# Performance work log

Hardware: AMD Instinct MI355X
Metric: run time of the kernel (lower is better)

Reference implementation:

```python
import jax, jax.numpy as jnp
import numpy as np

KH, KW = 7, 7            # full kernel after pad_w reflect of the (4,4) half-kernel
SIGMA_COLOR = 0.1


def extract_patches(x, kh, kw):
    """Per-pixel kh x kw neighborhoods with reflect padding.
    x: (B,C,H,W) -> (B,C,H,W,K) with K = kh*kw, k = i*kw + j (row-major),
    matching torch unfold(2,..).unfold(3,..).flatten(-2) ordering."""
    top, left = (kh - 1) // 2, (kw - 1) // 2
    xp = jnp.pad(x, ((0, 0), (0, 0), (top, kh - 1 - top), (left, kw - 1 - left)), mode='reflect')
    B, C, H, W = x.shape
    return jnp.stack([xp[:, :, i:i + H, j:j + W] for i in range(kh) for j in range(kw)], axis=-1)


def setup_inputs() -> dict:
    key = jax.random.key(0)
    k1, k2, k3 = jax.random.split(key, 3)
    B, C, H, W = 2, 3, 512, 512
    x = jax.random.uniform(k1, (B, C, H, W), dtype=jnp.float32)
    guidance = jax.random.uniform(k2, (B, C, H, W), dtype=jnp.float32)
    # learnable half-kernel logits, one per pixel (num_boxes = H*W with box=(1,1))
    w0 = jax.random.normal(k3, (B, H * W, KH // 2 + 1, KW // 2 + 1), dtype=jnp.float32)
    return {"x": x, "guidance": guidance, "w0": w0}


def reference(x, guidance, w0):
    B, C, H, W = x.shape
    K = KH * KW
    # pad_w: reflect-pad the stored (4,4) half-kernel back to the full (7,7) kernel
    w = jnp.pad(w0, ((0, 0), (0, 0), (0, KH // 2), (0, KW // 2)), mode='reflect')
    # softmax over the flattened kernel taps, per pixel
    sw = jax.nn.softmax(w.reshape(B, H, W, K), axis=-1)                     # (B,H,W,K)
    # bilateral color kernel: squared L1(channel) distance patch-vs-center
    gp = extract_patches(guidance, KH, KW)                                  # (B,C,H,W,K)
    dist = jnp.square(jnp.abs(gp - guidance[..., None]).sum(axis=1))        # (B,H,W,K)
    color = jnp.nan_to_num(jnp.exp((-0.5 / SIGMA_COLOR ** 2) * dist), nan=0.0)
    wt = sw * color                                                         # (B,H,W,K)
    # weighted local average, normalized by total weight
    xp = extract_patches(x, KH, KW)                                         # (B,C,H,W,K)
    num = jnp.einsum('bchwk,bhwk->bchw', xp, wt)
    den = wt.sum(axis=-1)[:, None]                                          # (B,1,H,W)
    return (num / den).astype(jnp.float32)
```

## Files before the change

kernel.cpp:

```cpp
#include <hip/hip_runtime.h>

#define TILE_W 32
#define TILE_H 8
#define HALO 3
#define SW_ (TILE_W + 2*HALO)
#define SH_ (TILE_H + 2*HALO)
#define H_IMG 512
#define W_IMG 512
#define C_IMG 3

__device__ __forceinline__ int reflect_idx(int q, int n) {
    q = (q < 0) ? -q : q;
    q = (q >= n) ? (2 * n - 2 - q) : q;
    return q;
}

__global__ __launch_bounds__(256) void AdaptiveFilter_71416716198124_kernel(
    const float* __restrict__ x,
    const float* __restrict__ g,
    const float* __restrict__ w0,
    float* __restrict__ out)
{
    __shared__ float sg[C_IMG][SH_][SW_];
    __shared__ float sx[C_IMG][SH_][SW_];

    const int b  = blockIdx.z;
    const int h0 = blockIdx.y * TILE_H;
    const int w0c = blockIdx.x * TILE_W;
    const int tid = threadIdx.y * TILE_W + threadIdx.x;

    const int plane = H_IMG * W_IMG;
    const float* gb = g + (size_t)b * C_IMG * plane;
    const float* xb = x + (size_t)b * C_IMG * plane;

    for (int idx = tid; idx < C_IMG * SH_ * SW_; idx += TILE_W * TILE_H) {
        int c = idx / (SH_ * SW_);
        int r = idx - c * (SH_ * SW_);
        int sh = r / SW_;
        int sw = r - sh * SW_;
        int gh = reflect_idx(h0 + sh - HALO, H_IMG);
        int gw = reflect_idx(w0c + sw - HALO, W_IMG);
        int off = c * plane + gh * W_IMG + gw;
        sg[c][sh][sw] = gb[off];
        sx[c][sh][sw] = xb[off];
    }
    __syncthreads();

    const int lx = threadIdx.x, ly = threadIdx.y;
    const int h = h0 + ly, w = w0c + lx;

    const float4* wp = (const float4*)(w0 + ((size_t)((b * plane) + h * W_IMG + w) << 4));
    float4 a0 = wp[0], a1 = wp[1], a2 = wp[2], a3 = wp[3];
    float wv[16] = {a0.x, a0.y, a0.z, a0.w, a1.x, a1.y, a1.z, a1.w,
                    a2.x, a2.y, a2.z, a2.w, a3.x, a3.y, a3.z, a3.w};
    float mx = wv[0];
    #pragma unroll
    for (int i = 1; i < 16; i++) mx = fmaxf(mx, wv[i]);

    const float gc0 = sg[0][ly + HALO][lx + HALO];
    const float gc1 = sg[1][ly + HALO][lx + HALO];
    const float gc2 = sg[2][ly + HALO][lx + HALO];

    float n0 = 0.f, n1 = 0.f, n2 = 0.f, den = 0.f;
    #pragma unroll
    for (int i = 0; i < 7; i++) {
        const int mi = (i < 4) ? i : 6 - i;
        #pragma unroll
        for (int j = 0; j < 7; j++) {
            const int mj = (j < 4) ? j : 6 - j;
            float d0 = fabsf(sg[0][ly + i][lx + j] - gc0);
            float d1 = fabsf(sg[1][ly + i][lx + j] - gc1);
            float d2 = fabsf(sg[2][ly + i][lx + j] - gc2);
            float s = d0 + d1 + d2;
            float wt = __expf(wv[mi * 4 + mj] - mx - 50.0f * (s * s));
            n0 = fmaf(sx[0][ly + i][lx + j], wt, n0);
            n1 = fmaf(sx[1][ly + i][lx + j], wt, n1);
            n2 = fmaf(sx[2][ly + i][lx + j], wt, n2);
            den += wt;
        }
    }
    const float inv = 1.0f / den;
    size_t ob = (size_t)b * C_IMG * plane + (size_t)h * W_IMG + w;
    out[ob]             = n0 * inv;
    out[ob + plane]     = n1 * inv;
    out[ob + 2 * plane] = n2 * inv;
}

extern "C" void kernel_launch(void* const* d_in, const int* in_sizes, int n_in,
                              void* d_out, int out_size, void* d_ws, size_t ws_size,
                              hipStream_t stream) {
    const float* x  = (const float*)d_in[0];
    const float* g  = (const float*)d_in[1];
    const float* w0 = (const float*)d_in[2];
    float* out = (float*)d_out;

    dim3 block(TILE_W, TILE_H, 1);
    dim3 grid(W_IMG / TILE_W, H_IMG / TILE_H, 2);
    AdaptiveFilter_71416716198124_kernel<<<grid, block, 0, stream>>>(x, g, w0, out);
}
```

Measured before the change: 94.41 us.

## Compute four horizontal pixels per thread with vectorized shared-memory row reuse

Each thread now produces four adjacent output pixels instead of one. For each kernel row it loads 12 contiguous guidance and input values per channel from shared memory as float4s and reuses them across the four pixels' 7 taps, then writes the outputs as float4. The tile becomes 64x16 with a padded 72-wide shared row, and the max subtraction is folded into the logits before the loop. This cuts LDS traffic and instruction count per pixel. In exchange it raises register pressure and leaves fewer blocks to fill the GPU. The per-thread w0 loads are now strided by 64 bytes across lanes, which may hurt coalescing.

```diff
diff --git a/kernel.cpp b/kernel.cpp
--- a/kernel.cpp
+++ b/kernel.cpp
@@ -1,13 +1,16 @@
 #include <hip/hip_runtime.h>
 
-#define TILE_W 32
-#define TILE_H 8
+#define TPX 4
+#define BX 16
+#define BY 16
+#define TILE_W (BX*TPX)
+#define TILE_H BY
 #define HALO 3
-#define SW_ (TILE_W + 2*HALO)
-#define SH_ (TILE_H + 2*HALO)
+#define SW_V (TILE_W + 2*HALO)
+#define SROW 72
+#define SH_T (TILE_H + 2*HALO)
 #define H_IMG 512
 #define W_IMG 512
-#define C_IMG 3
 
 __device__ __forceinline__ int reflect_idx(int q, int n) {
     q = (q < 0) ? -q : q;
@@ -21,23 +24,22 @@
     const float* __restrict__ w0,
     float* __restrict__ out)
 {
-    __shared__ float sg[C_IMG][SH_][SW_];
-    __shared__ float sx[C_IMG][SH_][SW_];
+    __shared__ __align__(16) float sg[3][SH_T][SROW];
+    __shared__ __align__(16) float sx[3][SH_T][SROW];
 
-    const int b  = blockIdx.z;
-    const int h0 = blockIdx.y * TILE_H;
+    const int b   = blockIdx.z;
+    const int h0  = blockIdx.y * TILE_H;
     const int w0c = blockIdx.x * TILE_W;
-    const int tid = threadIdx.y * TILE_W + threadIdx.x;
+    const int tid = threadIdx.y * BX + threadIdx.x;
+    const int plane = H_IMG * W_IMG;
+    const float* gb = g + (size_t)b * 3 * plane;
+    const float* xb = x + (size_t)b * 3 * plane;
 
-    const int plane = H_IMG * W_IMG;
-    const float* gb = g + (size_t)b * C_IMG * plane;
-    const float* xb = x + (size_t)b * C_IMG * plane;
-
-    for (int idx = tid; idx < C_IMG * SH_ * SW_; idx += TILE_W * TILE_H) {
-        int c = idx / (SH_ * SW_);
-        int r = idx - c * (SH_ * SW_);
-        int sh = r / SW_;
-        int sw = r - sh * SW_;
+    for (int idx = tid; idx < 3 * SH_T * SW_V; idx += BX * BY) {
+        int c  = idx / (SH_T * SW_V);
+        int r  = idx - c * (SH_T * SW_V);
+        int sh = r / SW_V;
+        int sw = r - sh * SW_V;
         int gh = reflect_idx(h0 + sh - HALO, H_IMG);
         int gw = reflect_idx(w0c + sw - HALO, W_IMG);
         int off = c * plane + gh * W_IMG + gw;
@@ -46,44 +48,106 @@
     }
     __syncthreads();
 
-    const int lx = threadIdx.x, ly = threadIdx.y;
-    const int h = h0 + ly, w = w0c + lx;
+    const int lx4 = threadIdx.x * TPX;
+    const int ly  = threadIdx.y;
+    const int h   = h0 + ly;
+    const int wb  = w0c + lx4;
 
-    const float4* wp = (const float4*)(w0 + ((size_t)((b * plane) + h * W_IMG + w) << 4));
-    float4 a0 = wp[0], a1 = wp[1], a2 = wp[2], a3 = wp[3];
-    float wv[16] = {a0.x, a0.y, a0.z, a0.w, a1.x, a1.y, a1.z, a1.w,
-                    a2.x, a2.y, a2.z, a2.w, a3.x, a3.y, a3.z, a3.w};
-    float mx = wv[0];
+    float lw[TPX][16];
     #pragma unroll
-    for (int i = 1; i < 16; i++) mx = fmaxf(mx, wv[i]);
+    for (int p = 0; p < TPX; p++) {
+        const float4* wp = (const float4*)(w0 +
+            (((size_t)b * plane + (size_t)h * W_IMG + (wb + p)) << 4));
+        float4 a0 = wp[0], a1 = wp[1], a2 = wp[2], a3 = wp[3];
+        float v[16] = {a0.x,a0.y,a0.z,a0.w, a1.x,a1.y,a1.z,a1.w,
+                       a2.x,a2.y,a2.z,a2.w, a3.x,a3.y,a3.z,a3.w};
+        float mx = v[0];
+        #pragma unroll
+        for (int k = 1; k < 16; k++) mx = fmaxf(mx, v[k]);
+        #pragma unroll
+        for (int k = 0; k < 16; k++) lw[p][k] = v[k] - mx;
+    }
 
-    const float gc0 = sg[0][ly + HALO][lx + HALO];
-    const float gc1 = sg[1][ly + HALO][lx + HALO];
-    const float gc2 = sg[2][ly + HALO][lx + HALO];
+    float gc[TPX][3];
+    #pragma unroll
+    for (int p = 0; p < TPX; p++)
+        #pragma unroll
+        for (int c = 0; c < 3; c++)
+            gc[p][c] = sg[c][ly + HALO][lx4 + HALO + p];
 
-    float n0 = 0.f, n1 = 0.f, n2 = 0.f, den = 0.f;
+    float acc[TPX][3] = {};
+    float den[TPX] = {};
+
     #pragma unroll
     for (int i = 0; i < 7; i++) {
-        const int mi = (i < 4) ? i : 6 - i;
+        const int mi4 = ((i < 4) ? i : 6 - i) * 4;
+
+        float sd[TPX][7];
         #pragma unroll
-        for (int j = 0; j < 7; j++) {
-            const int mj = (j < 4) ? j : 6 - j;
-            float d0 = fabsf(sg[0][ly + i][lx + j] - gc0);
-            float d1 = fabsf(sg[1][ly + i][lx + j] - gc1);
-            float d2 = fabsf(sg[2][ly + i][lx + j] - gc2);
-            float s = d0 + d1 + d2;
-            float wt = __expf(wv[mi * 4 + mj] - mx - 50.0f * (s * s));
-            n0 = fmaf(sx[0][ly + i][lx + j], wt, n0);
-            n1 = fmaf(sx[1][ly + i][lx + j], wt, n1);
-            n2 = fmaf(sx[2][ly + i][lx + j], wt, n2);
-            den += wt;
+        for (int p = 0; p < TPX; p++)
+            #pragma unroll
+            for (int j = 0; j < 7; j++) sd[p][j] = 0.f;
+
+        #pragma unroll
+        for (int c = 0; c < 3; c++) {
+            const float4* pg = (const float4*)&sg[c][ly + i][lx4];
+            float4 g0 = pg[0], g1 = pg[1], g2 = pg[2];
+            float rg[12] = {g0.x,g0.y,g0.z,g0.w, g1.x,g1.y,g1.z,g1.w,
+                            g2.x,g2.y,g2.z,g2.w};
+            #pragma unroll
+            for (int p = 0; p < TPX; p++) {
+                const float cc = gc[p][c];
+                #pragma unroll
+                for (int j = 0; j < 7; j++)
+                    sd[p][j] += fabsf(rg[p + j] - cc);
+            }
+        }
+
+        #pragma unroll
+        for (int p = 0; p < TPX; p++) {
+            #pragma unroll
+            for (int j = 0; j < 7; j++) {
+                const int mj = (j < 4) ? j : 6 - j;
+                const float s = sd[p][j];
+                sd[p][j] = __expf(fmaf(-50.0f * s, s, lw[p][mi4 + mj]));
+            }
+        }
+
+        #pragma unroll
+        for (int c = 0; c < 3; c++) {
+            const float4* px = (const float4*)&sx[c][ly + i][lx4];
+            float4 x0 = px[0], x1 = px[1], x2 = px[2];
+            float rx[12] = {x0.x,x0.y,x0.z,x0.w, x1.x,x1.y,x1.z,x1.w,
+                            x2.x,x2.y,x2.z,x2.w};
+            #pragma unroll
+            for (int p = 0; p < TPX; p++) {
+                float a = acc[p][c];
+                #pragma unroll
+                for (int j = 0; j < 7; j++)
+                    a = fmaf(rx[p + j], sd[p][j], a);
+                acc[p][c] = a;
+            }
+        }
+        #pragma unroll
+        for (int p = 0; p < TPX; p++) {
+            #pragma unroll
+            for (int j = 0; j < 7; j++) den[p] += sd[p][j];
         }
     }
-    const float inv = 1.0f / den;
-    size_t ob = (size_t)b * C_IMG * plane + (size_t)h * W_IMG + w;
-    out[ob]             = n0 * inv;
-    out[ob + plane]     = n1 * inv;
-    out[ob + 2 * plane] = n2 * inv;
+
+    float inv[TPX];
+    #pragma unroll
+    for (int p = 0; p < TPX; p++) inv[p] = 1.0f / den[p];
+
+    #pragma unroll
+    for (int c = 0; c < 3; c++) {
+        float4 o;
+        o.x = acc[0][c] * inv[0];
+        o.y = acc[1][c] * inv[1];
+        o.z = acc[2][c] * inv[2];
+        o.w = acc[3][c] * inv[3];
+        *(float4*)(out + (size_t)(b * 3 + c) * plane + (size_t)h * W_IMG + wb) = o;
+    }
 }
 
 extern "C" void kernel_launch(void* const* d_in, const int* in_sizes, int n_in,
@@ -94,7 +158,7 @@
     const float* w0 = (const float*)d_in[2];
     float* out = (float*)d_out;
 
-    dim3 block(TILE_W, TILE_H, 1);
+    dim3 block(BX, BY, 1);
     dim3 grid(W_IMG / TILE_W, H_IMG / TILE_H, 2);
     AdaptiveFilter_71416716198124_kernel<<<grid, block, 0, stream>>>(x, g, w0, out);
 }
```

After: 107.1 us. +13.5%, slower.
